# Kernel optimization log

Measured on AMD Instinct MI355X. Metric: run time of the kernel, lower is better.

The kernel has to match this reference:

```python
import jax, jax.numpy as jnp
import numpy as np

INPUT_DIM = 2048
NUM_EXPERTS = 64
TOP_K = 8
BATCH = 16384


def setup_inputs() -> dict:
    key = jax.random.key(0)
    k_x, k_n, k_wg, k_bg, k_wn = jax.random.split(key, 5)
    x = jax.random.normal(k_x, (BATCH, INPUT_DIM), dtype=jnp.float32)
    noise = jax.random.normal(k_n, (BATCH, NUM_EXPERTS), dtype=jnp.float32)
    Wg = jax.random.normal(k_wg, (NUM_EXPERTS, INPUT_DIM), dtype=jnp.float32) * 0.02
    bg = jax.random.normal(k_bg, (NUM_EXPERTS,), dtype=jnp.float32) * 0.02
    Wn = jax.random.normal(k_wn, (NUM_EXPERTS, INPUT_DIM), dtype=jnp.float32) * 0.02
    return {"x": x, "noise": noise, "Wg": Wg, "bg": bg, "Wn": Wn}


def reference(x, noise, Wg, bg, Wn):
    # logits: (B, E)
    logits = jnp.einsum("bd,ed->be", x, Wg) + bg
    noise_stddev = jax.nn.softplus(jnp.einsum("bd,ed->be", x, Wn))
    noisy_logits = logits + noise * noise_stddev

    top_k_values, top_k_indices = jax.lax.top_k(noisy_logits, TOP_K)  # (B, K)
    top_k_weights = jax.nn.softmax(top_k_values, axis=-1)

    # aux losses
    dispatch = jnp.argmax(noisy_logits, axis=-1)            # (B,)
    f = jax.nn.one_hot(dispatch, NUM_EXPERTS, dtype=logits.dtype).mean(axis=0)  # (E,)
    p = jax.nn.softmax(logits, axis=-1).mean(axis=0)        # (E,)
    load_balance_loss = NUM_EXPERTS * jnp.sum(f * p)
    z_loss = jnp.mean(jax.nn.logsumexp(logits, axis=-1) ** 2)

    return top_k_weights, top_k_indices, load_balance_loss, z_loss
```

## Files before the change

kernel.cpp:

```cpp
#include <hip/hip_runtime.h>
#include <math.h>

#define IDIM 2048
#define NE   64
#define TOPK 8
#define NB   16384
#define BM   32
#define BK   64
#define NCH  (IDIM / BK)
#define TAU  2.5e-4f

#define WS_CNT 129
#define WS_LIST 130
#define WSPLIT_BYTE 66560
#define WSPLIT_REQ  (WSPLIT_BYTE + NCH * 32768)

typedef __attribute__((ext_vector_type(8))) short bf16x8_t;
typedef __attribute__((ext_vector_type(4))) float f32x4_t;

__device__ __forceinline__ float softplusf(float v) {
    return (v > 0.f) ? (v + log1pf(expf(-v))) : log1pf(expf(v));
}
__device__ __forceinline__ double softplus_d(double v) {
    return (v > 0.0) ? (v + log1p(exp(-v))) : log1p(exp(v));
}

__device__ __forceinline__ short f2bf(float f) {
    unsigned u = __float_as_uint(f);
    unsigned r = (u + 0x7FFFu + ((u >> 16) & 1u)) >> 16;
    return (short)r;
}
__device__ __forceinline__ float bf2f(short s) {
    return __uint_as_float(((unsigned)(unsigned short)s) << 16);
}

__global__ void init_ws_kernel(float* ws) {
    int t = threadIdx.x;
    if (t < WS_LIST) ws[t] = 0.0f;
}

__device__ __forceinline__ void split8(const float4 v0, const float4 v1,
                                       bf16x8_t& H, bf16x8_t& L) {
    float fv[8] = {v0.x, v0.y, v0.z, v0.w, v1.x, v1.y, v1.z, v1.w};
    #pragma unroll
    for (int q = 0; q < 8; ++q) {
        short hb = f2bf(fv[q]);
        short lb = f2bf(fv[q] - bf2f(hb));
        H[q] = hb; L[q] = lb;
    }
}

__device__ __forceinline__ void cvt_slot(const float4 v0, const float4 v1,
                                         char* hiP, char* loP, int off) {
    bf16x8_t H, L;
    split8(v0, v1, H, L);
    *(bf16x8_t*)(hiP + off) = H;
    *(bf16x8_t*)(loP + off) = L;
}

__global__ __launch_bounds__(256) void prep_kernel(
    const float* __restrict__ Wg, const float* __restrict__ Wn,
    char* __restrict__ wsW, float* __restrict__ ws)
{
    if (blockIdx.x == 128) {
        if (threadIdx.x < WS_LIST) ws[threadIdx.x] = 0.0f;
        return;
    }
    int g = blockIdx.x * 256 + threadIdx.x;
    int t = g >> 10, i = g & 1023;
    int row = i >> 3, wslot = i & 7;
    int kslot = wslot ^ (row & 7);
    const float* src = (row < 64 ? Wg + (size_t)row * IDIM
                                 : Wn + (size_t)(row - 64) * IDIM) + t * BK + kslot * 8;
    float4 v0 = *(const float4*)src;
    float4 v1 = *(const float4*)(src + 4);
    bf16x8_t H, L;
    split8(v0, v1, H, L);
    char* dst = wsW + (size_t)t * 32768;
    *(bf16x8_t*)(dst + i * 16)         = H;
    *(bf16x8_t*)(dst + 16384 + i * 16) = L;
}

template<bool PRE>
__global__ __launch_bounds__(512, 4) void gate_main_kernel(
    const float* __restrict__ x, const float* __restrict__ noise,
    const float* __restrict__ Wg, const float* __restrict__ bg,
    const float* __restrict__ Wn, const char* __restrict__ wsW,
    float* __restrict__ out_w, float* __restrict__ out_i,
    float* __restrict__ ws, int listCap)
{
    __shared__ char smem[41488] __attribute__((aligned(16)));
    char* AH = smem;
    char* AL = smem + 4096;
    char* BH = smem + 8192;
    char* BL = smem + 24576;
    float* sP = (float*)(smem + 40960);
    float* sF = (float*)(smem + 41216);
    float* sZ = (float*)(smem + 41472);
    float* sL = (float*)smem;

    const int u   = threadIdx.x;
    const int w   = u >> 6;
    const int l   = u & 63;
    const int lr  = l & 15;
    const int lg4 = l >> 4;
    const int s7  = lr & 7;
    const int row0 = blockIdx.x * BM;

    if (u < NE) { sP[u] = 0.f; sF[u] = 0.f; }
    if (u == 0) sZ[0] = 0.f;

    const int ar  = (u >> 3) & 31;
    const int ac  = u & 7;
    const int aoff = ar * 128 + (((ac ^ (ar & 7)) & 7) << 4);
    const float* pa = x + (size_t)(row0 + ar) * IDIM + ac * 8;

    const int br  = u >> 3;
    const float* pg = Wg + (size_t)br * IDIM + ac * 8;
    const float* pn = Wn + (size_t)br * IDIM + ac * 8;
    const int woff = br * 128 + ((ac ^ (br & 7)) << 4);

    f32x4_t acc[2];
    #pragma unroll
    for (int mt = 0; mt < 2; ++mt) {
        f32x4_t z = {0.f, 0.f, 0.f, 0.f};
        acc[mt] = z;
    }

    float4 ra0, ra1;
    int4 w0, w1, w2, w3;
    float4 g0, g1, n0, n1;

#define LOADT(tt) { const int k0 = (tt) * BK;                                   \
    if (u < 256) { ra0 = *(const float4*)(pa + k0);                             \
                   ra1 = *(const float4*)(pa + k0 + 4); }                       \
    if constexpr (PRE) {                                                        \
        const char* s_ = wsW + (size_t)(tt) * 32768 + u * 16;                   \
        w0 = *(const int4*)(s_);          w1 = *(const int4*)(s_ + 8192);       \
        w2 = *(const int4*)(s_ + 16384);  w3 = *(const int4*)(s_ + 24576);      \
    } else {                                                                    \
        g0 = *(const float4*)(pg + k0);   g1 = *(const float4*)(pg + k0 + 4);   \
        n0 = *(const float4*)(pn + k0);   n1 = *(const float4*)(pn + k0 + 4);   \
    } }

    LOADT(0);

    for (int t = 0; t < NCH; ++t) {
        __syncthreads();
        if (u < 256) cvt_slot(ra0, ra1, AH, AL, aoff);
        if constexpr (PRE) {
            *(int4*)(BH + u * 16)        = w0;
            *(int4*)(BH + 8192 + u * 16) = w1;
            *(int4*)(BL + u * 16)        = w2;
            *(int4*)(BL + 8192 + u * 16) = w3;
        } else {
            cvt_slot(g0, g1, BH, BL, woff);
            cvt_slot(n0, n1, BH, BL, woff + 8192);
        }
        if (t + 1 < NCH) LOADT(t + 1);
        __syncthreads();

        #pragma unroll
        for (int ks = 0; ks < 2; ++ks) {
            const int so = (((ks * 4 + lg4) ^ s7) << 4);
            bf16x8_t ah[2], al_[2], bh, bl;
            #pragma unroll
            for (int mt = 0; mt < 2; ++mt) {
                const int o = (mt * 16 + lr) * 128 + so;
                ah[mt]  = *(const bf16x8_t*)(AH + o);
                al_[mt] = *(const bf16x8_t*)(AL + o);
            }
            {
                const int o = (w * 16 + lr) * 128 + so;
                bh = *(const bf16x8_t*)(BH + o);
                bl = *(const bf16x8_t*)(BL + o);
            }
            #pragma unroll
            for (int mt = 0; mt < 2; ++mt) {
                acc[mt] = __builtin_amdgcn_mfma_f32_16x16x32_bf16(ah[mt],  bh, acc[mt], 0, 0, 0);
                acc[mt] = __builtin_amdgcn_mfma_f32_16x16x32_bf16(ah[mt],  bl, acc[mt], 0, 0, 0);
                acc[mt] = __builtin_amdgcn_mfma_f32_16x16x32_bf16(al_[mt], bh, acc[mt], 0, 0, 0);
            }
        }
    }
    __syncthreads();

    #pragma unroll
    for (int mt = 0; mt < 2; ++mt)
        #pragma unroll
        for (int r = 0; r < 4; ++r)
            sL[(mt * 16 + lg4 * 4 + r) * 132 + (w * 16 + lr)] = acc[mt][r];
    __syncthreads();

    float pacc = 0.f, zacc = 0.f;
    #pragma unroll 1
    for (int rr = 0; rr < 4; ++rr) {
        const int r = w * 4 + rr;
        const int grow = row0 + r;
        float lg   = sL[r * 132 + l] + bg[l];
        float npre = sL[r * 132 + 64 + l];
        float vcur = fmaf(noise[(size_t)grow * NE + l], softplusf(npre), lg);

        float tkv[9]; int tki[9];
        #pragma unroll
        for (int k = 0; k < 9; ++k) {
            float mv = vcur; int mi = l;
            #pragma unroll
            for (int o = 32; o > 0; o >>= 1) {
                float ov = __shfl_xor(mv, o);
                int   oi = __shfl_xor(mi, o);
                if (ov > mv || (ov == mv && oi < mi)) { mv = ov; mi = oi; }
            }
            tkv[k] = mv; tki[k] = mi;
            if (l == mi) vcur = -1e30f;
        }

        float m0 = tkv[0], s = 0.f, wk[TOPK];
        #pragma unroll
        for (int k = 0; k < TOPK; ++k) { wk[k] = expf(tkv[k] - m0); s += wk[k]; }
        float inv = 1.f / s;
        float myw = 0.f; int myi = 0;
        #pragma unroll
        for (int k = 0; k < TOPK; ++k)
            if (l == k) { myw = wk[k] * inv; myi = tki[k]; }
        if (l < TOPK) {
            out_w[(size_t)grow * TOPK + l] = myw;
            out_i[(size_t)grow * TOPK + l] = (float)myi;
        }

        if (l == 0) {
            atomicAdd(&sF[tki[0]], 1.f);
            float ming = 1e30f;
            #pragma unroll
            for (int k = 0; k < 8; ++k) ming = fminf(ming, tkv[k] - tkv[k + 1]);
            if (ming < TAU) {
                int slot = atomicAdd((int*)&ws[WS_CNT], 1);
                if (slot < listCap) ((int*)ws)[WS_LIST + slot] = grow;
            }
        }

        float rm = lg;
        #pragma unroll
        for (int o = 32; o > 0; o >>= 1) rm = fmaxf(rm, __shfl_xor(rm, o));
        float pe = expf(lg - rm);
        float ssum = pe;
        #pragma unroll
        for (int o = 32; o > 0; o >>= 1) ssum += __shfl_xor(ssum, o);
        pacc += pe / ssum;
        if (l == 0) { float lse = rm + logf(ssum); zacc += lse * lse; }
    }

    atomicAdd(&sP[l], pacc);
    if (l == 0) atomicAdd(sZ, zacc);
    __syncthreads();
    if (u < NE) {
        atomicAdd(&ws[u],      sF[u]);
        atomicAdd(&ws[NE + u], sP[u]);
    }
    if (u == 0) atomicAdd(&ws[2 * NE], sZ[0]);
}

__global__ __launch_bounds__(512) void recheck_finalize_kernel(
    const float* __restrict__ x, const float* __restrict__ noise,
    const float* __restrict__ Wg, const float* __restrict__ bg,
    const float* __restrict__ Wn,
    float* __restrict__ out_w, float* __restrict__ out_i, float* __restrict__ out_s,
    const float* __restrict__ ws, int listCap)
{
    __shared__ double sRed[1024];
    const int t = threadIdx.x;

    if (blockIdx.x == 0 && t < 64) {
        float v = (ws[t] / (float)NB) * (ws[NE + t] / (float)NB);
        #pragma unroll
        for (int o = 32; o > 0; o >>= 1) v += __shfl_down(v, o);
        if (t == 0) {
            out_s[0] = (float)NE * v;
            out_s[1] = ws[2 * NE] / (float)NB;
        }
    }

    const int* wsi = (const int*)ws;
    int cnt = wsi[WS_CNT];
    if (cnt > listCap) cnt = listCap;
    if (cnt <= 0) return;

    const int slot = t & 127;
    const int q4   = t >> 7;
    const float* wrb = ((slot < 64) ? (Wg + (size_t)slot * IDIM)
                                    : (Wn + (size_t)(slot - 64) * IDIM)) + q4 * 512;

    const int npair = (cnt + 1) >> 1;
    for (int bi = blockIdx.x; bi < npair; bi += gridDim.x) {
        const int i1 = 2 * bi + 1;
        const int r0 = wsi[WS_LIST + 2 * bi];
        const int r1 = wsi[WS_LIST + (i1 < cnt ? i1 : cnt - 1)];
        const float* x0 = x + (size_t)r0 * IDIM + q4 * 512;
        const float* x1 = x + (size_t)r1 * IDIM + q4 * 512;

        double a0 = 0.0, a1 = 0.0;
        #pragma unroll 4
        for (int k = 0; k < 512; k += 4) {
            float4 wv  = *(const float4*)(wrb + k);
            float4 xv0 = *(const float4*)(x0 + k);
            float4 xv1 = *(const float4*)(x1 + k);
            a0 = fma((double)xv0.x, (double)wv.x, a0);
            a1 = fma((double)xv1.x, (double)wv.x, a1);
            a0 = fma((double)xv0.y, (double)wv.y, a0);
            a1 = fma((double)xv1.y, (double)wv.y, a1);
            a0 = fma((double)xv0.z, (double)wv.z, a0);
            a1 = fma((double)xv1.z, (double)wv.z, a1);
            a0 = fma((double)xv0.w, (double)wv.w, a0);
            a1 = fma((double)xv1.w, (double)wv.w, a1);
        }
        sRed[t * 2]     = a0;
        sRed[t * 2 + 1] = a1;
        __syncthreads();
        if (t < 128) {
            #pragma unroll
            for (int i = 0; i < 2; ++i)
                sRed[t * 2 + i] = sRed[t * 2 + i] + sRed[(t + 128) * 2 + i]
                                + sRed[(t + 256) * 2 + i] + sRed[(t + 384) * 2 + i];
        }
        __syncthreads();

        if (t < 64) {
            const int lane = t;
            const double bgl = (double)bg[lane];
            #pragma unroll 1
            for (int i = 0; i < 2; ++i) {
                const int row = i ? r1 : r0;
                double g = sRed[lane * 2 + i];
                double n = sRed[(64 + lane) * 2 + i];
                double lgd = g + bgl;
                double nz = (double)noise[(size_t)row * NE + lane];
                double vcur = fma(nz, softplus_d(n), lgd);

                double tkv[TOPK]; int tki[TOPK];
                #pragma unroll
                for (int k = 0; k < TOPK; ++k) {
                    double mv = vcur; int mi = lane;
                    #pragma unroll
                    for (int o = 32; o > 0; o >>= 1) {
                        double ov = __shfl_xor(mv, o);
                        int    oi = __shfl_xor(mi, o);
                        if (ov > mv || (ov == mv && oi < mi)) { mv = ov; mi = oi; }
                    }
                    tkv[k] = mv; tki[k] = mi;
                    if (lane == mi) vcur = -1e300;
                }
                double m0 = tkv[0], s = 0.0, wk[TOPK];
                #pragma unroll
                for (int k = 0; k < TOPK; ++k) { wk[k] = exp(tkv[k] - m0); s += wk[k]; }
                double inv = 1.0 / s;
                float myw = 0.f; int myi = 0;
                #pragma unroll
                for (int k = 0; k < TOPK; ++k)
                    if (lane == k) { myw = (float)(wk[k] * inv); myi = tki[k]; }
                if (lane < TOPK) {
                    out_w[(size_t)row * TOPK + lane] = myw;
                    out_i[(size_t)row * TOPK + lane] = (float)myi;
                }
            }
        }
        __syncthreads();
    }
}

extern "C" void kernel_launch(void* const* d_in, const int* in_sizes, int n_in,
                              void* d_out, int out_size, void* d_ws, size_t ws_size,
                              hipStream_t stream) {
    const float* x     = (const float*)d_in[0];
    const float* noise = (const float*)d_in[1];
    const float* Wg    = (const float*)d_in[2];
    const float* bg    = (const float*)d_in[3];
    const float* Wn    = (const float*)d_in[4];
    float* out = (float*)d_out;
    float* ws  = (float*)d_ws;
    char*  wsW = (char*)d_ws + WSPLIT_BYTE;

    long cap = (long)(ws_size / 4) - WS_LIST;
    int listCap = (int)(cap < 0 ? 0 : (cap > NB ? NB : cap));
    const bool pre = ws_size >= (size_t)WSPLIT_REQ;

    if (pre) {
        hipLaunchKernelGGL(prep_kernel, dim3(129), dim3(256), 0, stream, Wg, Wn, wsW, ws);
        hipLaunchKernelGGL(gate_main_kernel<true>, dim3(NB / BM), dim3(512), 0, stream,
                           x, noise, Wg, bg, Wn, wsW,
                           out, out + (size_t)NB * TOPK, ws, listCap);
    } else {
        hipLaunchKernelGGL(init_ws_kernel, dim3(1), dim3(256), 0, stream, ws);
        hipLaunchKernelGGL(gate_main_kernel<false>, dim3(NB / BM), dim3(512), 0, stream,
                           x, noise, Wg, bg, Wn, wsW,
                           out, out + (size_t)NB * TOPK, ws, listCap);
    }
    hipLaunchKernelGGL(recheck_finalize_kernel, dim3(1024), dim3(512), 0, stream,
                       x, noise, Wg, bg, Wn,
                       out, out + (size_t)NB * TOPK, out + 2 * (size_t)NB * TOPK,
                       ws, listCap);
}
```

Before: 142.2 us.

## Split GEMM over K halves into separate kernel and move gating to its own pass

Adds a path that splits the x·W reduction into two K halves, each handled by its own block, so the grid has twice as many blocks and the GEMM phase is better parallelised. Partial sums are written to workspace and a separate gating kernel adds them, applies softplus noise, top-k, softmax and the aux-loss accumulation. This trades extra global traffic of about 16 MB for the partials plus an extra kernel launch for higher occupancy and simpler GEMM blocks. The path is used only when the workspace is large enough.

```diff
diff --git a/kernel.cpp b/kernel.cpp
--- a/kernel.cpp
+++ b/kernel.cpp
@@ -8,12 +8,17 @@
 #define BM   32
 #define BK   64
 #define NCH  (IDIM / BK)
+#define KH   1024
+#define NCHH 16
 #define TAU  2.5e-4f
 
 #define WS_CNT 129
 #define WS_LIST 130
 #define WSPLIT_BYTE 66560
 #define WSPLIT_REQ  (WSPLIT_BYTE + NCH * 32768)
+#define PART0_BYTE  (WSPLIT_BYTE + NCH * 32768)
+#define PART1_BYTE  (PART0_BYTE + (size_t)NB * 128 * 4)
+#define SPLIT_REQ   (PART1_BYTE + (size_t)NB * 128 * 4)
 
 typedef __attribute__((ext_vector_type(8))) short bf16x8_t;
 typedef __attribute__((ext_vector_type(4))) float f32x4_t;
@@ -79,6 +84,175 @@
     char* dst = wsW + (size_t)t * 32768;
     *(bf16x8_t*)(dst + i * 16)         = H;
     *(bf16x8_t*)(dst + 16384 + i * 16) = L;
+}
+
+__global__ __launch_bounds__(512, 4) void gemm_half_kernel(
+    const float* __restrict__ x, const char* __restrict__ wsW,
+    float* __restrict__ part0, float* __restrict__ part1)
+{
+    __shared__ char smem[40960] __attribute__((aligned(16)));
+    char* AH = smem;
+    char* AL = smem + 4096;
+    char* BH = smem + 8192;
+    char* BL = smem + 24576;
+
+    const int u   = threadIdx.x;
+    const int w   = u >> 6;
+    const int l   = u & 63;
+    const int lr  = l & 15;
+    const int lg4 = l >> 4;
+    const int s7  = lr & 7;
+    const int half = blockIdx.x & 1;
+    const int row0 = (blockIdx.x >> 1) * BM;
+    float* pb = half ? part1 : part0;
+
+    const int ar  = (u >> 3) & 31;
+    const int ac  = u & 7;
+    const int aoff = ar * 128 + (((ac ^ (ar & 7)) & 7) << 4);
+    const float* pa = x + (size_t)(row0 + ar) * IDIM + half * KH + ac * 8;
+
+    f32x4_t acc[2];
+    #pragma unroll
+    for (int mt = 0; mt < 2; ++mt) {
+        f32x4_t z = {0.f, 0.f, 0.f, 0.f};
+        acc[mt] = z;
+    }
+
+    float4 ra0, ra1;
+    int4 w0, w1, w2, w3;
+
+#define HLOADT(tt) { const int k0 = (tt) * BK;                                  \
+    if (u < 256) { ra0 = *(const float4*)(pa + k0);                             \
+                   ra1 = *(const float4*)(pa + k0 + 4); }                       \
+    const char* s_ = wsW + (size_t)(half * NCHH + (tt)) * 32768 + u * 16;       \
+    w0 = *(const int4*)(s_);          w1 = *(const int4*)(s_ + 8192);           \
+    w2 = *(const int4*)(s_ + 16384);  w3 = *(const int4*)(s_ + 24576); }
+
+    HLOADT(0);
+
+    for (int t = 0; t < NCHH; ++t) {
+        __syncthreads();
+        if (u < 256) cvt_slot(ra0, ra1, AH, AL, aoff);
+        *(int4*)(BH + u * 16)        = w0;
+        *(int4*)(BH + 8192 + u * 16) = w1;
+        *(int4*)(BL + u * 16)        = w2;
+        *(int4*)(BL + 8192 + u * 16) = w3;
+        if (t + 1 < NCHH) HLOADT(t + 1);
+        __syncthreads();
+
+        #pragma unroll
+        for (int ks = 0; ks < 2; ++ks) {
+            const int so = (((ks * 4 + lg4) ^ s7) << 4);
+            bf16x8_t ah[2], al_[2], bh, bl;
+            #pragma unroll
+            for (int mt = 0; mt < 2; ++mt) {
+                const int o = (mt * 16 + lr) * 128 + so;
+                ah[mt]  = *(const bf16x8_t*)(AH + o);
+                al_[mt] = *(const bf16x8_t*)(AL + o);
+            }
+            {
+                const int o = (w * 16 + lr) * 128 + so;
+                bh = *(const bf16x8_t*)(BH + o);
+                bl = *(const bf16x8_t*)(BL + o);
+            }
+            #pragma unroll
+            for (int mt = 0; mt < 2; ++mt) {
+                acc[mt] = __builtin_amdgcn_mfma_f32_16x16x32_bf16(ah[mt],  bh, acc[mt], 0, 0, 0);
+                acc[mt] = __builtin_amdgcn_mfma_f32_16x16x32_bf16(ah[mt],  bl, acc[mt], 0, 0, 0);
+                acc[mt] = __builtin_amdgcn_mfma_f32_16x16x32_bf16(al_[mt], bh, acc[mt], 0, 0, 0);
+            }
+        }
+    }
+
+    #pragma unroll
+    for (int mt = 0; mt < 2; ++mt)
+        #pragma unroll
+        for (int r = 0; r < 4; ++r)
+            pb[(size_t)(row0 + mt * 16 + lg4 * 4 + r) * 128 + (w * 16 + lr)] = acc[mt][r];
+}
+
+__global__ __launch_bounds__(512) void gating_kernel(
+    const float* __restrict__ part0, const float* __restrict__ part1,
+    const float* __restrict__ noise, const float* __restrict__ bg,
+    float* __restrict__ out_w, float* __restrict__ out_i,
+    float* __restrict__ ws, int listCap)
+{
+    __shared__ float sP[NE];
+    __shared__ float sF[NE];
+    __shared__ float sZ[1];
+    const int u = threadIdx.x;
+    const int w = u >> 6, l = u & 63;
+    const int row0 = blockIdx.x * 128;
+
+    if (u < NE) { sP[u] = 0.f; sF[u] = 0.f; }
+    if (u == 0) sZ[0] = 0.f;
+    __syncthreads();
+
+    float pacc = 0.f, zacc = 0.f;
+    #pragma unroll 1
+    for (int rr = 0; rr < 16; ++rr) {
+        const int grow = row0 + w * 16 + rr;
+        float lg   = part0[(size_t)grow * 128 + l] + part1[(size_t)grow * 128 + l] + bg[l];
+        float npre = part0[(size_t)grow * 128 + 64 + l] + part1[(size_t)grow * 128 + 64 + l];
+        float vcur = fmaf(noise[(size_t)grow * NE + l], softplusf(npre), lg);
+
+        float tkv[9]; int tki[9];
+        #pragma unroll
+        for (int k = 0; k < 9; ++k) {
+            float mv = vcur; int mi = l;
+            #pragma unroll
+            for (int o = 32; o > 0; o >>= 1) {
+                float ov = __shfl_xor(mv, o);
+                int   oi = __shfl_xor(mi, o);
+                if (ov > mv || (ov == mv && oi < mi)) { mv = ov; mi = oi; }
+            }
+            tkv[k] = mv; tki[k] = mi;
+            if (l == mi) vcur = -1e30f;
+        }
+
+        float m0 = tkv[0], s = 0.f, wk[TOPK];
+        #pragma unroll
+        for (int k = 0; k < TOPK; ++k) { wk[k] = expf(tkv[k] - m0); s += wk[k]; }
+        float inv = 1.f / s;
+        float myw = 0.f; int myi = 0;
+        #pragma unroll
+        for (int k = 0; k < TOPK; ++k)
+            if (l == k) { myw = wk[k] * inv; myi = tki[k]; }
+        if (l < TOPK) {
+            out_w[(size_t)grow * TOPK + l] = myw;
+            out_i[(size_t)grow * TOPK + l] = (float)myi;
+        }
+
+        if (l == 0) {
+            atomicAdd(&sF[tki[0]], 1.f);
+            float ming = 1e30f;
+            #pragma unroll
+            for (int k = 0; k < 8; ++k) ming = fminf(ming, tkv[k] - tkv[k + 1]);
+            if (ming < TAU) {
+                int slot = atomicAdd((int*)&ws[WS_CNT], 1);
+                if (slot < listCap) ((int*)ws)[WS_LIST + slot] = grow;
+            }
+        }
+
+        float rm = lg;
+        #pragma unroll
+        for (int o = 32; o > 0; o >>= 1) rm = fmaxf(rm, __shfl_xor(rm, o));
+        float pe = expf(lg - rm);
+        float ssum = pe;
+        #pragma unroll
+        for (int o = 32; o > 0; o >>= 1) ssum += __shfl_xor(ssum, o);
+        pacc += pe / ssum;
+        if (l == 0) { float lse = rm + logf(ssum); zacc += lse * lse; }
+    }
+
+    atomicAdd(&sP[l], pacc);
+    if (l == 0) atomicAdd(sZ, zacc);
+    __syncthreads();
+    if (u < NE) {
+        atomicAdd(&ws[u],      sF[u]);
+        atomicAdd(&ws[NE + u], sP[u]);
+    }
+    if (u == 0) atomicAdd(&ws[2 * NE], sZ[0]);
 }
 
 template<bool PRE>
@@ -381,9 +555,19 @@
 
     long cap = (long)(ws_size / 4) - WS_LIST;
     int listCap = (int)(cap < 0 ? 0 : (cap > NB ? NB : cap));
-    const bool pre = ws_size >= (size_t)WSPLIT_REQ;
-
-    if (pre) {
+    const bool pre   = ws_size >= (size_t)WSPLIT_REQ;
+    const bool split = ws_size >= (size_t)SPLIT_REQ;
+
+    if (split) {
+        float* part0 = (float*)((char*)d_ws + PART0_BYTE);
+        float* part1 = (float*)((char*)d_ws + PART1_BYTE);
+        hipLaunchKernelGGL(prep_kernel, dim3(129), dim3(256), 0, stream, Wg, Wn, wsW, ws);
+        hipLaunchKernelGGL(gemm_half_kernel, dim3(2 * NB / BM), dim3(512), 0, stream,
+                           x, wsW, part0, part1);
+        hipLaunchKernelGGL(gating_kernel, dim3(NB / 128), dim3(512), 0, stream,
+                           part0, part1, noise, bg,
+                           out, out + (size_t)NB * TOPK, ws, listCap);
+    } else if (pre) {
         hipLaunchKernelGGL(prep_kernel, dim3(129), dim3(256), 0, stream, Wg, Wn, wsW, ws);
         hipLaunchKernelGGL(gate_main_kernel<true>, dim3(NB / BM), dim3(512), 0, stream,
                            x, noise, Wg, bg, Wn, wsW,
```

New measurement: 208.5 us. 1.47x slower.
